# Kernel tuning notes

Measured on AMD Instinct MI355X. Metric: run time of the kernel, lower is better.

The kernel has to match this reference:

```python
import jax, jax.numpy as jnp
import numpy as np

N_NODES = 20000
N_EDGES = 160000
B = 200      # num graphs (nodes per graph = 100)
T = 8        # num_tau
A = 10       # action_size
H = 4        # heads
D = 128      # out_channels
R = 4        # num_relations
NCOS = 64


def rgat(x, edge_index, edge_type, W, q, k, b):
    # W: [R, in, H*D]; q, k: [H*D, H]; b: [D]
    xw = jnp.einsum('ni,rio->nro', x, W)              # [N, R, H*D]
    src, dst = edge_index[0], edge_index[1]
    xj = xw[src, edge_type]                            # [E, H*D] gather by edge + relation
    xi = xw[dst, edge_type]                            # [E, H*D]
    alpha = jax.nn.leaky_relu(xi @ q + xj @ k, 0.2)    # [E, H]
    amax = jax.ops.segment_max(alpha, dst, num_segments=N_NODES)
    ex = jnp.exp(alpha - amax[dst])                    # segment softmax over dst
    denom = jax.ops.segment_sum(ex, dst, num_segments=N_NODES)
    a = ex / denom[dst]                                # [E, H]
    msg = (a[:, :, None] * xj.reshape(-1, H, D)).reshape(-1, H * D)
    agg = jax.ops.segment_sum(msg, dst, num_segments=N_NODES).reshape(-1, H, D)
    return agg.mean(axis=1) + b                        # concat=False -> mean over heads


def noisy_linear(z, w, bias, sw, sb, ew, eb):
    # torch convention: w [out, in]
    return z @ (w + sw * ew).T + (bias + sb * eb)


def setup_inputs():
    key = jax.random.key(0)
    ks = jax.random.split(key, 48)
    def rn(i, shape, scale=0.05):
        return jax.random.normal(ks[i], shape, dtype=jnp.float32) * scale
    SIG = 0.017
    inp = {
        'x': jax.random.normal(ks[0], (N_NODES, 2), dtype=jnp.float32),
        'edge_index': jax.random.randint(ks[1], (2, N_EDGES), 0, N_NODES, dtype=jnp.int32),
        'edge_type': jax.random.randint(ks[2], (N_EDGES,), 0, R, dtype=jnp.int32),
        'taus': jax.random.uniform(ks[3], (B, T, 1), dtype=jnp.float32),
        'W1': rn(4, (R, 2, H * D), 0.3), 'q1': rn(5, (H * D, H), 0.05), 'k1': rn(6, (H * D, H), 0.05), 'b1': rn(7, (D,)),
        'W2': rn(8, (R, D, H * D), 0.06), 'q2': rn(9, (H * D, H), 0.05), 'k2': rn(10, (H * D, H), 0.05), 'b2': rn(11, (D,)),
        'cos_w': rn(12, (D, NCOS), 0.1), 'cos_b': rn(13, (D,)),
        'ff1_w': rn(14, (D, D), 0.1), 'ff1_b': rn(15, (D,)),
        'ff1_sw': jnp.full((D, D), SIG, jnp.float32), 'ff1_sb': jnp.full((D,), SIG, jnp.float32),
        'ff1_ew': rn(16, (D, D), 1.0), 'ff1_eb': rn(17, (D,), 1.0),
        'ff2_w': rn(18, (D, D), 0.1), 'ff2_b': rn(19, (D,)),
        'ff2_sw': jnp.full((D, D), SIG, jnp.float32), 'ff2_sb': jnp.full((D,), SIG, jnp.float32),
        'ff2_ew': rn(20, (D, D), 1.0), 'ff2_eb': rn(21, (D,), 1.0),
        'adv_w': rn(22, (A, D), 0.1), 'adv_b': rn(23, (A,)),
        'adv_sw': jnp.full((A, D), SIG, jnp.float32), 'adv_sb': jnp.full((A,), SIG, jnp.float32),
        'adv_ew': rn(24, (A, D), 1.0), 'adv_eb': rn(25, (A,), 1.0),
        'val_w': rn(26, (1, D), 0.1), 'val_b': rn(27, (1,)),
        'val_sw': jnp.full((1, D), SIG, jnp.float32), 'val_sb': jnp.full((1,), SIG, jnp.float32),
        'val_ew': rn(28, (1, D), 1.0), 'val_eb': rn(29, (1,), 1.0),
    }
    return inp


def reference(x, edge_index, edge_type, taus,
              W1, q1, k1, b1, W2, q2, k2, b2, cos_w, cos_b,
              ff1_w, ff1_b, ff1_sw, ff1_sb, ff1_ew, ff1_eb,
              ff2_w, ff2_b, ff2_sw, ff2_sb, ff2_ew, ff2_eb,
              adv_w, adv_b, adv_sw, adv_sb, adv_ew, adv_eb,
              val_w, val_b, val_sw, val_sb, val_ew, val_eb):
    h = jax.nn.selu(rgat(x, edge_index, edge_type, W1, q1, k1, b1))
    h = jax.nn.selu(rgat(h, edge_index, edge_type, W2, q2, k2, b2))
    g = h.reshape(B, N_NODES // B, D).sum(axis=1)      # global_add_pool (block batch_idx)
    pis = jnp.pi * jnp.arange(1, NCOS + 1, dtype=jnp.float32)  # [NCOS]
    cos = jnp.cos(taus * pis)                           # [B, T, NCOS]
    cos_x = jax.nn.relu(cos @ cos_w.T + cos_b)          # [B, T, D]
    z = (g[:, None, :] * cos_x).reshape(B * T, D)
    z = jax.nn.selu(noisy_linear(z, ff1_w, ff1_b, ff1_sw, ff1_sb, ff1_ew, ff1_eb))
    z = jax.nn.selu(noisy_linear(z, ff2_w, ff2_b, ff2_sw, ff2_sb, ff2_ew, ff2_eb))
    adv = noisy_linear(z, adv_w, adv_b, adv_sw, adv_sb, adv_ew, adv_eb)   # [B*T, A]
    val = noisy_linear(z, val_w, val_b, val_sw, val_sb, val_ew, val_eb)   # [B*T, 1]
    out = val + adv - adv.mean(axis=1, keepdims=True)
    return out.reshape(B, T, A), taus
```

## Files before the change

### kernel.cpp

```cpp
#include <hip/hip_runtime.h>
#include <hip/hip_bf16.h>

constexpr long NN = 20000;
constexpr long NE = 160000;
constexpr long BB = 200;
constexpr long TT = 8;
constexpr long GN = 100;

constexpr long O_FLAG = 0;
constexpr long O_X    = 16;                 constexpr long N_X   = 40000;
constexpr long O_TAU  = O_X + N_X;          constexpr long N_TAU = 1600;
constexpr long O_W1   = O_TAU + N_TAU;      constexpr long N_W1  = 4096;
constexpr long O_Q1   = O_W1 + N_W1;        constexpr long N_Q   = 2048;
constexpr long O_K1   = O_Q1 + N_Q;
constexpr long O_B1   = O_K1 + N_Q;         constexpr long N_B   = 128;
constexpr long O_W2   = O_B1 + N_B;         constexpr long N_W2  = 262144;
constexpr long O_Q2   = O_W2 + N_W2;
constexpr long O_K2   = O_Q2 + N_Q;
constexpr long O_B2   = O_K2 + N_Q;
constexpr long O_CW   = O_B2 + N_B;         constexpr long N_CW  = 8192;
constexpr long O_CB   = O_CW + N_CW;
constexpr long O_F1W  = O_CB + N_B;         constexpr long N_FW  = 16384;
constexpr long O_F1B  = O_F1W + N_FW;
constexpr long O_F1SW = O_F1B + N_B;
constexpr long O_F1SB = O_F1SW + N_FW;
constexpr long O_F1EW = O_F1SB + N_B;
constexpr long O_F1EB = O_F1EW + N_FW;
constexpr long O_F2W  = O_F1EB + N_B;
constexpr long O_F2B  = O_F2W + N_FW;
constexpr long O_F2SW = O_F2B + N_B;
constexpr long O_F2SB = O_F2SW + N_FW;
constexpr long O_F2EW = O_F2SB + N_B;
constexpr long O_F2EB = O_F2EW + N_FW;
constexpr long O_AW   = O_F2EB + N_B;       constexpr long N_AW  = 1280;
constexpr long O_AB   = O_AW + N_AW;        constexpr long N_AB  = 16;
constexpr long O_ASW  = O_AB + N_AB;
constexpr long O_ASB  = O_ASW + N_AW;
constexpr long O_AEW  = O_ASB + N_AB;
constexpr long O_AEB  = O_AEW + N_AW;
constexpr long O_VW   = O_AEB + N_AB;       constexpr long N_VW  = 128;
constexpr long O_VB   = O_VW + N_VW;        constexpr long N_VB  = 16;
constexpr long O_VSW  = O_VB + N_VB;
constexpr long O_VSB  = O_VSW + N_VW;
constexpr long O_VEW  = O_VSB + N_VB;
constexpr long O_VEB  = O_VEW + N_VW;
constexpr long O_WQ1  = O_VEB + N_VB;
constexpr long O_WK1  = O_WQ1 + 32;
constexpr long O_WQ2  = O_WK1 + 32;
constexpr long O_WK2  = O_WQ2 + 2048;
constexpr long O_CF1W = O_WK2 + 2048;
constexpr long O_CF1B = O_CF1W + N_FW;
constexpr long O_CF2W = O_CF1B + N_B;
constexpr long O_CF2B = O_CF2W + N_FW;
constexpr long O_CAW  = O_CF2B + N_B;
constexpr long O_CAB  = O_CAW + N_AW;
constexpr long O_CVW  = O_CAB + N_AB;
constexpr long O_CVB  = O_CVW + N_VW;
constexpr long O_AL1  = O_CVB + N_VB;
constexpr long O_AL2  = O_AL1 + NE*4;
constexpr long O_H1   = O_AL2 + NE*4;
constexpr long O_H2   = O_H1 + NN*128;
constexpr long O_G    = O_H2 + NN*128;
constexpr long O_Z0   = O_G + BB*128;
constexpr long O_Z1   = O_Z0 + BB*TT*128;
constexpr long O_Z2   = O_Z1 + BB*TT*128;
constexpr long O_AGG1 = O_Z2 + BB*TT*128;
constexpr long O_DEG  = O_AGG1;
constexpr long O_CUR  = O_DEG + NN;
constexpr long O_ROWP = O_CUR + NN;
constexpr long O_PERM = O_ROWP + NN + 8;
constexpr long O_XW2  = O_AGG1 + NN*128 + NN*128 + NN*16;
constexpr long O_END_TABLE = O_XW2 + (NN*4*512)/2;
constexpr long MPAD   = 20096;
constexpr long O_H1B  = O_END_TABLE;
constexpr long O_W2BT = O_H1B + (MPAD*128)/2;
constexpr long O_END2 = O_W2BT + (2048L*128)/2;
constexpr long O_AQ   = O_END2;
constexpr long O_AK   = O_AQ + NN*16;
constexpr long O_END3 = O_AK + NN*16;

#define DEVFN __device__ __forceinline__

typedef __attribute__((ext_vector_type(8))) short bf16x8;
typedef __attribute__((ext_vector_type(4))) float f32x4;
typedef __attribute__((ext_vector_type(8))) unsigned short u16x8;

DEVFN float selu_f(float x){ return 1.0507009873554805f * (x > 0.f ? x : 1.6732632423543772f * expm1f(x)); }
DEVFN float lrelu_f(float x){ return x >= 0.f ? x : 0.2f * x; }
DEVFN float bf2f(unsigned short u){ return __uint_as_float(((unsigned)u) << 16); }
DEVFN float wred_max(float v){
    #pragma unroll
    for (int off = 32; off > 0; off >>= 1) v = fmaxf(v, __shfl_xor(v, off));
    return v;
}
DEVFN float wred_sum(float v){
    #pragma unroll
    for (int off = 32; off > 0; off >>= 1) v += __shfl_xor(v, off);
    return v;
}
DEVFN unsigned short f2bfu(float x){
    __hip_bfloat16 b = __float2bfloat16(x);
    return *(unsigned short*)&b;
}

__global__ void k_pre(const unsigned short* taus_u16, const int* ei, float* ws){
    if (blockIdx.x == 0){
        if (threadIdx.x == 0){
            int bf = 1;
            for (int i = 0; i < 128; i++) if (taus_u16[i] > 0x3F80u){ bf = 0; break; }
            ((int*)ws)[0] = bf;
        }
        return;
    }
    long e = (long)(blockIdx.x - 1)*blockDim.x + threadIdx.x;
    if (e >= NE) return;
    atomicAdd((int*)(ws + O_DEG) + ei[NE + e], 1);
}

__global__ void k_scan(float* ws){
    const int* deg = (const int*)(ws + O_DEG);
    int* rowp = (int*)(ws + O_ROWP);
    __shared__ int part[256];
    int tid = threadIdx.x;
    int base = tid * 79;
    int n = 0; if (base < NN) n = min(79, (int)NN - base);
    int s = 0;
    for (int i = 0; i < n; i++) s += deg[base + i];
    part[tid] = s;
    __syncthreads();
    if (tid == 0){
        int acc = 0;
        for (int i = 0; i < 256; i++){ int t = part[i]; part[i] = acc; acc += t; }
    }
    __syncthreads();
    int acc = part[tid];
    for (int i = 0; i < n; i++){ rowp[base + i] = acc; acc += deg[base + i]; }
    if (tid == 0) rowp[NN] = (int)NE;
}

struct ConvArgs { const void* src[38]; long off[38]; int n[38]; };

__global__ void k_conv_scatter(ConvArgs a, const int* ei, float* ws){
    int y = blockIdx.y;
    if (y == 38){
        long e = (long)blockIdx.x*blockDim.x + threadIdx.x;
        if (e >= NE) return;
        int dst = ei[NE + e];
        int pos = atomicAdd((int*)(ws + O_CUR) + dst, 1);
        ((int*)(ws + O_PERM))[((const int*)(ws + O_ROWP))[dst] + pos] = (int)e;
        return;
    }
    long off = a.off[y];
    if (off < 0) return;
    const void* s = a.src[y];
    int n = a.n[y];
    int bf = ((const int*)ws)[0];
    for (int i = blockIdx.x*blockDim.x + threadIdx.x; i < n; i += gridDim.x*blockDim.x){
        float v;
        if (bf){ unsigned short u = ((const unsigned short*)s)[i]; v = bf2f(u); }
        else   { v = ((const float*)s)[i]; }
        ws[off + i] = v;
    }
}

__global__ void k_prep(float* ws){
    int phase = blockIdx.y;
    int idx = blockIdx.x*blockDim.x + threadIdx.x;
    if (phase == 0){
        if (idx >= 4160) return;
        long wsrc, qsrc, dst; int ri, h;
        if (idx < 64){
            int t = idx & 31; h = t & 3; ri = t >> 2;
            wsrc = O_W1 + (long)ri*512;
            qsrc = (idx < 32) ? O_Q1 : O_K1;
            dst  = ((idx < 32) ? O_WQ1 : O_WK1) + t;
        } else {
            int t = (idx - 64) & 2047; h = t & 3; ri = t >> 2;
            wsrc = O_W2 + (long)ri*512;
            qsrc = (idx < 2112) ? O_Q2 : O_K2;
            dst  = ((idx < 2112) ? O_WQ2 : O_WK2) + t;
        }
        const float* W = ws + wsrc;
        const float* Q = ws + qsrc;
        float s = 0.f;
        for (int o = 0; o < 512; o++) s += W[o] * Q[o*4 + h];
        ws[dst] = s;
    } else if (phase == 1){
        const long tw[8] = {O_F1W,O_F2W,O_AW,O_VW, O_F1B,O_F2B,O_AB,O_VB};
        const long ts[8] = {O_F1SW,O_F2SW,O_ASW,O_VSW, O_F1SB,O_F2SB,O_ASB,O_VSB};
        const long te[8] = {O_F1EW,O_F2EW,O_AEW,O_VEW, O_F1EB,O_F2EB,O_AEB,O_VEB};
        const long td[8] = {O_CF1W,O_CF2W,O_CAW,O_CVW, O_CF1B,O_CF2B,O_CAB,O_CVB};
        const int  tn[8] = {16384,16384,1280,128, 128,128,10,1};
        const int  tb[8] = {0,16384,32768,34048, 34176,34304,34432,34442};
        int total = 34443;
        for (int i = idx; i < total; i += gridDim.x*blockDim.x){
            int t = 0;
            #pragma unroll
            for (int q = 1; q < 8; q++) if (i >= tb[q]) t = q;
            int j = i - tb[t];
            if (j < tn[t]) ws[td[t] + j] = ws[tw[t] + j] + ws[ts[t] + j]*ws[te[t] + j];
        }
    } else if (phase == 2){
        if (idx >= 262144) return;
        int np = idx & 2047, k = idx >> 11;
        int r = np >> 9, q = np & 511, d = q >> 2, h = q & 3;
        float v = ws[O_W2 + (long)r*65536 + (long)k*512 + h*128 + d];
        ((__hip_bfloat16*)(ws + O_W2BT))[(long)np*128 + k] = __float2bfloat16(v);
    } else {
        if (idx < 6144) ws[O_H1B + (20000L*128)/2 + idx] = 0.f;
    }
}

__global__ __launch_bounds__(256) void k_node1(const int* ei, const int* et, float* ws){
    int wid = threadIdx.x >> 6, lane = threadIdx.x & 63;
    long n = (long)blockIdx.x*4 + wid;
    const int* rowp = (const int*)(ws + O_ROWP);
    const int* perm = (const int*)(ws + O_PERM);
    int e0 = rowp[n], deg = rowp[n+1] - e0;
    float xd0 = ws[O_X + n*2], xd1 = ws[O_X + n*2 + 1];
    bool have = lane < deg;
    float al[4], xs0 = 0.f, xs1 = 0.f; int rt0 = 0;
    float mx[4] = {-3.0e38f,-3.0e38f,-3.0e38f,-3.0e38f};
    if (have){
        int e = perm[e0 + lane]; int src = ei[e]; rt0 = et[e];
        xs0 = ws[O_X + (long)src*2]; xs1 = ws[O_X + (long)src*2 + 1];
        const float* Wq = ws + O_WQ1 + rt0*8;
        const float* Wk = ws + O_WK1 + rt0*8;
        #pragma unroll
        for (int h = 0; h < 4; h++){
            al[h] = lrelu_f(xd0*Wq[h] + xd1*Wq[4+h] + xs0*Wk[h] + xs1*Wk[4+h]);
            mx[h] = al[h];
        }
    }
    for (int j0 = 64; j0 < deg; j0 += 64){
        int j = j0 + lane;
        if (j < deg){
            int e = perm[e0 + j]; int src = ei[e]; int rt = et[e];
            float a0 = ws[O_X + (long)src*2], a1 = ws[O_X + (long)src*2 + 1];
            const float* Wq = ws + O_WQ1 + rt*8;
            const float* Wk = ws + O_WK1 + rt*8;
            #pragma unroll
            for (int h = 0; h < 4; h++)
                mx[h] = fmaxf(mx[h], lrelu_f(xd0*Wq[h] + xd1*Wq[4+h] + a0*Wk[h] + a1*Wk[4+h]));
        }
    }
    #pragma unroll
    for (int h = 0; h < 4; h++) mx[h] = wred_max(mx[h]);
    float s[4][4][2];
    #pragma unroll
    for (int r = 0; r < 4; r++)
        #pragma unroll
        for (int h = 0; h < 4; h++){ s[r][h][0] = 0.f; s[r][h][1] = 0.f; }
    float den[4] = {0.f,0.f,0.f,0.f};
    if (have){
        #pragma unroll
        for (int h = 0; h < 4; h++){
            float ex = expf(al[h] - mx[h]);
            den[h] += ex;
            float c0 = ex*xs0, c1 = ex*xs1;
            #pragma unroll
            for (int r = 0; r < 4; r++){
                if (r == rt0){ s[r][h][0] += c0; s[r][h][1] += c1; }
            }
        }
    }
    for (int j0 = 64; j0 < deg; j0 += 64){
        int j = j0 + lane;
        if (j < deg){
            int e = perm[e0 + j]; int src = ei[e]; int rt = et[e];
            float a0 = ws[O_X + (long)src*2], a1 = ws[O_X + (long)src*2 + 1];
            const float* Wq = ws + O_WQ1 + rt*8;
            const float* Wk = ws + O_WK1 + rt*8;
            #pragma unroll
            for (int h = 0; h < 4; h++){
                float a = lrelu_f(xd0*Wq[h] + xd1*Wq[4+h] + a0*Wk[h] + a1*Wk[4+h]);
                float ex = expf(a - mx[h]);
                den[h] += ex;
                float c0 = ex*a0, c1 = ex*a1;
                #pragma unroll
                for (int r = 0; r < 4; r++){
                    if (r == rt){ s[r][h][0] += c0; s[r][h][1] += c1; }
                }
            }
        }
    }
    #pragma unroll
    for (int h = 0; h < 4; h++) den[h] = wred_sum(den[h]);
    #pragma unroll
    for (int r = 0; r < 4; r++)
        #pragma unroll
        for (int h = 0; h < 4; h++){
            s[r][h][0] = wred_sum(s[r][h][0]);
            s[r][h][1] = wred_sum(s[r][h][1]);
        }
    float rden[4];
    #pragma unroll
    for (int h = 0; h < 4; h++) rden[h] = den[h] > 0.f ? 0.25f/den[h] : 0.f;
    float v0 = 0.f, v1 = 0.f;
    #pragma unroll
    for (int r = 0; r < 4; r++)
        #pragma unroll
        for (int h = 0; h < 4; h++){
            float2 wa = *(const float2*)&ws[O_W1 + r*1024 +       h*128 + lane*2];
            float2 wb = *(const float2*)&ws[O_W1 + r*1024 + 512 + h*128 + lane*2];
            float t0 = s[r][h][0]*rden[h], t1 = s[r][h][1]*rden[h];
            v0 += wa.x*t0 + wb.x*t1;
            v1 += wa.y*t0 + wb.y*t1;
        }
    float2 b2 = *(const float2*)&ws[O_B1 + lane*2];
    float o0 = selu_f(v0 + b2.x), o1 = selu_f(v1 + b2.y);
    unsigned short* p = (unsigned short*)(ws + O_H1B) + n*128 + lane*2;
    ushort2 pk; pk.x = f2bfu(o0); pk.y = f2bfu(o1);
    *(ushort2*)p = pk;
}

__global__ void k_aqk(float* ws){
    __shared__ float wq[128*16];
    __shared__ float wk[128*16];
    __shared__ float hl[16][129];
    int tid = threadIdx.x;
    long nb = (long)blockIdx.x * 16;
    const unsigned short* h1b = (const unsigned short*)(ws + O_H1B);
    #pragma unroll
    for (int c = 0; c < 8; c++){
        int idx = tid + c*256;
        int i = idx >> 4, o = idx & 15;
        int r = o >> 2, h = o & 3;
        wq[i*16 + o] = ws[O_WQ2 + r*512 + i*4 + h];
        wk[i*16 + o] = ws[O_WK2 + r*512 + i*4 + h];
        hl[idx >> 7][idx & 127] = bf2f(h1b[nb*128 + idx]);
    }
    __syncthreads();
    int j = tid >> 4, o = tid & 15;
    float aq = 0.f, ak = 0.f;
    #pragma unroll 4
    for (int i = 0; i < 128; i++){
        float hv = hl[j][i];
        aq += hv * wq[i*16 + o];
        ak += hv * wk[i*16 + o];
    }
    ws[O_AQ + (nb + j)*16 + o] = aq;
    ws[O_AK + (nb + j)*16 + o] = ak;
}

__global__ void k_xw2_mfma(float* ws){
    __shared__ __align__(16) unsigned short Ash[128*128];
    __shared__ __align__(16) unsigned short Bsh[128*128];
    const unsigned short* h1b  = (const unsigned short*)(ws + O_H1B);
    const unsigned short* w2bt = (const unsigned short*)(ws + O_W2BT);
    long bm = (long)blockIdx.x * 128;
    long bn = (long)blockIdx.y * 128;
    int tid = threadIdx.x;
    char* Ac = (char*)Ash; char* Bc = (char*)Bsh;
    #pragma unroll
    for (int i = 0; i < 8; i++){
        int c = tid + i*256;
        int row = c >> 4, kb = (c & 15) * 16;
        int off = row*256 + (kb ^ ((row & 7) << 4));
        *(bf16x8*)(Ac + off) = *(const bf16x8*)&h1b [(bm + row)*128 + (c & 15)*8];
        *(bf16x8*)(Bc + off) = *(const bf16x8*)&w2bt[(bn + row)*128 + (c & 15)*8];
    }
    __syncthreads();
    int w = tid >> 6, lane = tid & 63;
    int wm = (w >> 1) * 64, wn = (w & 1) * 64;
    int r16 = lane & 15, kq = lane >> 4;
    f32x4 acc[4][4] = {};
    #pragma unroll
    for (int ks = 0; ks < 4; ks++){
        int kbyte = ks*64 + kq*16;
        bf16x8 a[4], b[4];
        #pragma unroll
        for (int m = 0; m < 4; m++){
            int row = wm + m*16 + r16;
            a[m] = *(const bf16x8*)(Ac + row*256 + (kbyte ^ ((row & 7) << 4)));
        }
        #pragma unroll
        for (int n = 0; n < 4; n++){
            int row = wn + n*16 + r16;
            b[n] = *(const bf16x8*)(Bc + row*256 + (kbyte ^ ((row & 7) << 4)));
        }
        #pragma unroll
        for (int m = 0; m < 4; m++)
            #pragma unroll
            for (int n = 0; n < 4; n++)
                acc[m][n] = __builtin_amdgcn_mfma_f32_16x16x32_bf16(a[m], b[n], acc[m][n], 0, 0, 0);
    }
    __hip_bfloat16* xb = (__hip_bfloat16*)(ws + O_XW2);
    #pragma unroll
    for (int m = 0; m < 4; m++){
        long gr0 = bm + wm + m*16 + kq*4;
        #pragma unroll
        for (int j = 0; j < 4; j++){
            long gr = gr0 + j;
            if (gr < NN){
                #pragma unroll
                for (int n = 0; n < 4; n++){
                    long gc = bn + wn + n*16 + r16;
                    xb[gr*2048 + gc] = __float2bfloat16(acc[m][n][j]);
                }
            }
        }
    }
}

__global__ __launch_bounds__(256) void k_node2(const int* ei, const int* et, float* ws){
    __shared__ float excs[4][64][4];
    __shared__ int   esrts[4][64];
    int wid = threadIdx.x >> 6, lane = threadIdx.x & 63;
    long n = (long)blockIdx.x*4 + wid;
    const int* rowp = (const int*)(ws + O_ROWP);
    const int* perm = (const int*)(ws + O_PERM);
    int e0 = rowp[n], deg = rowp[n+1] - e0;
    bool have = lane < deg;
    float al[4]; int srt = 0;
    float mx[4] = {-3.0e38f,-3.0e38f,-3.0e38f,-3.0e38f};
    if (have){
        int e = perm[e0 + lane]; int src = ei[e]; int rt = et[e]; srt = src*4 + rt;
        float4 q4 = *(const float4*)&ws[O_AQ + n*16 + rt*4];
        float4 k4 = *(const float4*)&ws[O_AK + (long)src*16 + rt*4];
        al[0] = lrelu_f(q4.x + k4.x); al[1] = lrelu_f(q4.y + k4.y);
        al[2] = lrelu_f(q4.z + k4.z); al[3] = lrelu_f(q4.w + k4.w);
        #pragma unroll
        for (int h = 0; h < 4; h++) mx[h] = al[h];
    }
    for (int j0 = 64; j0 < deg; j0 += 64){
        int j = j0 + lane;
        if (j < deg){
            int e = perm[e0 + j]; int src = ei[e]; int rt = et[e];
            float4 q4 = *(const float4*)&ws[O_AQ + n*16 + rt*4];
            float4 k4 = *(const float4*)&ws[O_AK + (long)src*16 + rt*4];
            mx[0] = fmaxf(mx[0], lrelu_f(q4.x + k4.x));
            mx[1] = fmaxf(mx[1], lrelu_f(q4.y + k4.y));
            mx[2] = fmaxf(mx[2], lrelu_f(q4.z + k4.z));
            mx[3] = fmaxf(mx[3], lrelu_f(q4.w + k4.w));
        }
    }
    #pragma unroll
    for (int h = 0; h < 4; h++) mx[h] = wred_max(mx[h]);
    float den[4] = {0.f,0.f,0.f,0.f};
    if (have){
        #pragma unroll
        for (int h = 0; h < 4; h++){
            float ex = expf(al[h] - mx[h]);
            den[h] += ex;
            excs[wid][lane][h] = ex;
        }
        esrts[wid][lane] = srt;
    }
    for (int j0 = 64; j0 < deg; j0 += 64){
        int j = j0 + lane;
        if (j < deg){
            int e = perm[e0 + j]; int src = ei[e]; int rt = et[e];
            float4 q4 = *(const float4*)&ws[O_AQ + n*16 + rt*4];
            float4 k4 = *(const float4*)&ws[O_AK + (long)src*16 + rt*4];
            den[0] += expf(lrelu_f(q4.x + k4.x) - mx[0]);
            den[1] += expf(lrelu_f(q4.y + k4.y) - mx[1]);
            den[2] += expf(lrelu_f(q4.z + k4.z) - mx[2]);
            den[3] += expf(lrelu_f(q4.w + k4.w) - mx[3]);
        }
    }
    #pragma unroll
    for (int h = 0; h < 4; h++) den[h] = wred_sum(den[h]);
    __syncthreads();
    const unsigned short* xw2 = (const unsigned short*)(ws + O_XW2);
    float a0[4] = {0.f,0.f,0.f,0.f}, a1[4] = {0.f,0.f,0.f,0.f};
    int mdeg = min(deg, 64);
    int j = 0;
    for (; j + 4 <= mdeg; j += 4){
        long s0 = esrts[wid][j], s1 = esrts[wid][j+1], s2 = esrts[wid][j+2], s3 = esrts[wid][j+3];
        u16x8 v0 = *(const u16x8*)(xw2 + s0*512 + lane*8);
        u16x8 v1 = *(const u16x8*)(xw2 + s1*512 + lane*8);
        u16x8 v2 = *(const u16x8*)(xw2 + s2*512 + lane*8);
        u16x8 v3 = *(const u16x8*)(xw2 + s3*512 + lane*8);
        #pragma unroll
        for (int h = 0; h < 4; h++){
            a0[h] += excs[wid][j  ][h]*bf2f(v0[h]); a1[h] += excs[wid][j  ][h]*bf2f(v0[4+h]);
            a0[h] += excs[wid][j+1][h]*bf2f(v1[h]); a1[h] += excs[wid][j+1][h]*bf2f(v1[4+h]);
            a0[h] += excs[wid][j+2][h]*bf2f(v2[h]); a1[h] += excs[wid][j+2][h]*bf2f(v2[4+h]);
            a0[h] += excs[wid][j+3][h]*bf2f(v3[h]); a1[h] += excs[wid][j+3][h]*bf2f(v3[4+h]);
        }
    }
    for (; j < mdeg; j++){
        long sr = esrts[wid][j];
        u16x8 v = *(const u16x8*)(xw2 + sr*512 + lane*8);
        #pragma unroll
        for (int h = 0; h < 4; h++){
            a0[h] += excs[wid][j][h]*bf2f(v[h]);
            a1[h] += excs[wid][j][h]*bf2f(v[4+h]);
        }
    }
    for (j = 64; j < deg; j++){
        int e = perm[e0 + j]; int src = ei[e]; int rt = et[e];
        float4 q4 = *(const float4*)&ws[O_AQ + n*16 + rt*4];
        float4 k4 = *(const float4*)&ws[O_AK + (long)src*16 + rt*4];
        float ex[4];
        ex[0] = expf(lrelu_f(q4.x + k4.x) - mx[0]);
        ex[1] = expf(lrelu_f(q4.y + k4.y) - mx[1]);
        ex[2] = expf(lrelu_f(q4.z + k4.z) - mx[2]);
        ex[3] = expf(lrelu_f(q4.w + k4.w) - mx[3]);
        u16x8 v = *(const u16x8*)(xw2 + ((long)src*4 + rt)*512 + lane*8);
        #pragma unroll
        for (int h = 0; h < 4; h++){
            a0[h] += ex[h]*bf2f(v[h]);
            a1[h] += ex[h]*bf2f(v[4+h]);
        }
    }
    float rd[4];
    #pragma unroll
    for (int h = 0; h < 4; h++) rd[h] = den[h] > 0.f ? 0.25f/den[h] : 0.f;
    float o0 = a0[0]*rd[0] + a0[1]*rd[1] + a0[2]*rd[2] + a0[3]*rd[3];
    float o1 = a1[0]*rd[0] + a1[1]*rd[1] + a1[2]*rd[2] + a1[3]*rd[3];
    float2 b2 = *(const float2*)&ws[O_B2 + lane*2];
    float2 outv; outv.x = selu_f(o0 + b2.x); outv.y = selu_f(o1 + b2.y);
    *(float2*)&ws[O_H2 + n*128 + lane*2] = outv;
}

__global__ void k_pool(float* ws){
    int b = blockIdx.x, d = threadIdx.x;
    float s = 0.f;
    for (int j = 0; j < GN; j++) s += ws[O_H2 + ((long)b*GN + j)*128 + d];
    ws[O_G + (long)b*128 + d] = s;
}

__global__ void k_tail(float* ws, void* d_out, const void* taus_raw){
    __shared__ float cs[64];
    __shared__ float row0[128], row1[128], row2[128];
    __shared__ float advs[12];
    int bt = blockIdx.x, t = threadIdx.x;
    int b = bt >> 3;
    if (t < 64){
        float tau = ws[O_TAU + bt];
        cs[t] = cosf(tau * (3.14159265358979323846f * (float)(t + 1)));
    }
    __syncthreads();
    {
        const float* cw = ws + O_CW + (long)t*64;
        float s = ws[O_CB + t];
        for (int c = 0; c < 64; c++) s += cs[c]*cw[c];
        s = fmaxf(s, 0.f);
        row0[t] = ws[O_G + (long)b*128 + t] * s;
    }
    __syncthreads();
    {
        const float* W = ws + O_CF1W + (long)t*128;
        float s = ws[O_CF1B + t];
        for (int i = 0; i < 128; i++) s += row0[i]*W[i];
        row1[t] = selu_f(s);
    }
    __syncthreads();
    {
        const float* W = ws + O_CF2W + (long)t*128;
        float s = ws[O_CF2B + t];
        for (int i = 0; i < 128; i++) s += row1[i]*W[i];
        row2[t] = selu_f(s);
    }
    __syncthreads();
    if (t < 11){
        const float* W = (t < 10) ? (ws + O_CAW + (long)t*128) : (ws + O_CVW);
        float s = (t < 10) ? ws[O_CAB + t] : ws[O_CVB];
        for (int i = 0; i < 128; i++) s += row2[i]*W[i];
        advs[t] = s;
    }
    __syncthreads();
    if (t == 0){
        float m = 0.f;
        #pragma unroll
        for (int a = 0; a < 10; a++) m += advs[a];
        m *= 0.1f;
        float val = advs[10];
        int bf = ((const int*)ws)[0];
        if (bf){
            __hip_bfloat16* out = (__hip_bfloat16*)d_out;
            for (int a = 0; a < 10; a++) out[(long)bt*10 + a] = __float2bfloat16(val + advs[a] - m);
            ((unsigned short*)d_out)[16000 + bt] = ((const unsigned short*)taus_raw)[bt];
        } else {
            float* out = (float*)d_out;
            for (int a = 0; a < 10; a++) out[(long)bt*10 + a] = val + advs[a] - m;
            out[16000 + bt] = ((const float*)taus_raw)[bt];
        }
    }
}

extern "C" void kernel_launch(void* const* d_in, const int* in_sizes, int n_in,
                              void* d_out, int out_size, void* d_ws, size_t ws_size,
                              hipStream_t stream){
    (void)in_sizes; (void)n_in; (void)out_size; (void)ws_size;
    float* ws = (float*)d_ws;
    const int* ei = (const int*)d_in[1];
    const int* et = (const int*)d_in[2];

    hipMemsetAsync(ws + O_DEG, 0, (size_t)(2*NN)*4, stream);

    k_pre<<<626, 256, 0, stream>>>((const unsigned short*)d_in[3], ei, ws);
    k_scan<<<1, 256, 0, stream>>>(ws);

    ConvArgs ca;
    static const long conv_o[38] = {
        O_X, -1, -1, O_TAU, O_W1, O_Q1, O_K1, O_B1, O_W2, O_Q2, O_K2, O_B2, O_CW, O_CB,
        O_F1W, O_F1B, O_F1SW, O_F1SB, O_F1EW, O_F1EB,
        O_F2W, O_F2B, O_F2SW, O_F2SB, O_F2EW, O_F2EB,
        O_AW, O_AB, O_ASW, O_ASB, O_AEW, O_AEB,
        O_VW, O_VB, O_VSW, O_VSB, O_VEW, O_VEB };
    static const int conv_n[38] = {
        40000, 0, 0, 1600, 4096, 2048, 2048, 128, 262144, 2048, 2048, 128, 8192, 128,
        16384, 128, 16384, 128, 16384, 128,
        16384, 128, 16384, 128, 16384, 128,
        1280, 10, 1280, 10, 1280, 10,
        128, 1, 128, 1, 128, 1 };
    for (int i = 0; i < 38; i++){ ca.src[i] = d_in[i]; ca.off[i] = conv_o[i]; ca.n[i] = conv_n[i]; }
    k_conv_scatter<<<dim3(625, 39), 256, 0, stream>>>(ca, ei, ws);

    k_prep<<<dim3(1024, 4), 256, 0, stream>>>(ws);

    k_node1<<<5000, 256, 0, stream>>>(ei, et, ws);

    k_xw2_mfma<<<dim3(157, 16), 256, 0, stream>>>(ws);
    k_aqk<<<1250, 256, 0, stream>>>(ws);
    k_node2<<<5000, 256, 0, stream>>>(ei, et, ws);

    k_pool<<<200, 128, 0, stream>>>(ws);
    k_tail<<<1600, 128, 0, stream>>>(ws, d_out, d_in[3]);
}
```

Baseline: 260.6 us.

## Map 16 lanes per node in RGAT node kernels instead of one wavefront

Both node aggregation kernels now process 16 nodes per 256-thread block, with 16 lanes per node instead of a full 64-lane wave. Average in-degree is about 8, so most lanes of a wave sat idle before. In layer 1 the per-relation sums go into shared-memory atomics instead of register arrays plus full-wave reductions. In layer 2 the softmax normalisation is folded into the per-edge weights, and each lane accumulates 8 output dims from wider row loads. The cost is more work per lane, shared atomics, and reliance on wave-synchronous ordering of shared memory with no explicit barriers.

```diff
diff --git a/kernel.cpp b/kernel.cpp
--- a/kernel.cpp
+++ b/kernel.cpp
@@ -88,19 +88,19 @@
 DEVFN float selu_f(float x){ return 1.0507009873554805f * (x > 0.f ? x : 1.6732632423543772f * expm1f(x)); }
 DEVFN float lrelu_f(float x){ return x >= 0.f ? x : 0.2f * x; }
 DEVFN float bf2f(unsigned short u){ return __uint_as_float(((unsigned)u) << 16); }
-DEVFN float wred_max(float v){
-    #pragma unroll
-    for (int off = 32; off > 0; off >>= 1) v = fmaxf(v, __shfl_xor(v, off));
-    return v;
-}
-DEVFN float wred_sum(float v){
-    #pragma unroll
-    for (int off = 32; off > 0; off >>= 1) v += __shfl_xor(v, off);
-    return v;
-}
 DEVFN unsigned short f2bfu(float x){
     __hip_bfloat16 b = __float2bfloat16(x);
     return *(unsigned short*)&b;
+}
+DEVFN float g16_max(float v){
+    #pragma unroll
+    for (int off = 8; off > 0; off >>= 1) v = fmaxf(v, __shfl_xor(v, off));
+    return v;
+}
+DEVFN float g16_sum(float v){
+    #pragma unroll
+    for (int off = 8; off > 0; off >>= 1) v += __shfl_xor(v, off);
+    return v;
 }
 
 __global__ void k_pre(const unsigned short* taus_u16, const int* ei, float* ws){
@@ -212,17 +212,20 @@
 }
 
 __global__ __launch_bounds__(256) void k_node1(const int* ei, const int* et, float* ws){
-    int wid = threadIdx.x >> 6, lane = threadIdx.x & 63;
-    long n = (long)blockIdx.x*4 + wid;
+    __shared__ float sacc[16][32];
+    int tid = threadIdx.x;
+    int g = tid >> 4, t = tid & 15;
+    long n = (long)blockIdx.x*16 + g;
+    sacc[g][t] = 0.f; sacc[g][t + 16] = 0.f;
     const int* rowp = (const int*)(ws + O_ROWP);
     const int* perm = (const int*)(ws + O_PERM);
     int e0 = rowp[n], deg = rowp[n+1] - e0;
     float xd0 = ws[O_X + n*2], xd1 = ws[O_X + n*2 + 1];
-    bool have = lane < deg;
+    bool have = t < deg;
     float al[4], xs0 = 0.f, xs1 = 0.f; int rt0 = 0;
     float mx[4] = {-3.0e38f,-3.0e38f,-3.0e38f,-3.0e38f};
     if (have){
-        int e = perm[e0 + lane]; int src = ei[e]; rt0 = et[e];
+        int e = perm[e0 + t]; int src = ei[e]; rt0 = et[e];
         xs0 = ws[O_X + (long)src*2]; xs1 = ws[O_X + (long)src*2 + 1];
         const float* Wq = ws + O_WQ1 + rt0*8;
         const float* Wk = ws + O_WK1 + rt0*8;
@@ -232,8 +235,8 @@
             mx[h] = al[h];
         }
     }
-    for (int j0 = 64; j0 < deg; j0 += 64){
-        int j = j0 + lane;
+    for (int j0 = 16; j0 < deg; j0 += 16){
+        int j = j0 + t;
         if (j < deg){
             int e = perm[e0 + j]; int src = ei[e]; int rt = et[e];
             float a0 = ws[O_X + (long)src*2], a1 = ws[O_X + (long)src*2 + 1];
@@ -245,27 +248,19 @@
         }
     }
     #pragma unroll
-    for (int h = 0; h < 4; h++) mx[h] = wred_max(mx[h]);
-    float s[4][4][2];
-    #pragma unroll
-    for (int r = 0; r < 4; r++)
-        #pragma unroll
-        for (int h = 0; h < 4; h++){ s[r][h][0] = 0.f; s[r][h][1] = 0.f; }
+    for (int h = 0; h < 4; h++) mx[h] = g16_max(mx[h]);
     float den[4] = {0.f,0.f,0.f,0.f};
     if (have){
         #pragma unroll
         for (int h = 0; h < 4; h++){
             float ex = expf(al[h] - mx[h]);
-            den[h] += ex;
-            float c0 = ex*xs0, c1 = ex*xs1;
-            #pragma unroll
-            for (int r = 0; r < 4; r++){
-                if (r == rt0){ s[r][h][0] += c0; s[r][h][1] += c1; }
-            }
-        }
-    }
-    for (int j0 = 64; j0 < deg; j0 += 64){
-        int j = j0 + lane;
+            den[h] = ex;
+            atomicAdd(&sacc[g][rt0*8 + h*2 + 0], ex*xs0);
+            atomicAdd(&sacc[g][rt0*8 + h*2 + 1], ex*xs1);
+        }
+    }
+    for (int j0 = 16; j0 < deg; j0 += 16){
+        int j = j0 + t;
         if (j < deg){
             int e = perm[e0 + j]; int src = ei[e]; int rt = et[e];
             float a0 = ws[O_X + (long)src*2], a1 = ws[O_X + (long)src*2 + 1];
@@ -276,42 +271,41 @@
                 float a = lrelu_f(xd0*Wq[h] + xd1*Wq[4+h] + a0*Wk[h] + a1*Wk[4+h]);
                 float ex = expf(a - mx[h]);
                 den[h] += ex;
-                float c0 = ex*a0, c1 = ex*a1;
-                #pragma unroll
-                for (int r = 0; r < 4; r++){
-                    if (r == rt){ s[r][h][0] += c0; s[r][h][1] += c1; }
-                }
+                atomicAdd(&sacc[g][rt*8 + h*2 + 0], ex*a0);
+                atomicAdd(&sacc[g][rt*8 + h*2 + 1], ex*a1);
             }
         }
     }
     #pragma unroll
-    for (int h = 0; h < 4; h++) den[h] = wred_sum(den[h]);
+    for (int h = 0; h < 4; h++) den[h] = g16_sum(den[h]);
+    float rden[4];
+    #pragma unroll
+    for (int h = 0; h < 4; h++) rden[h] = den[h] > 0.f ? 0.25f/den[h] : 0.f;
+    float v[8];
+    #pragma unroll
+    for (int k = 0; k < 8; k++) v[k] = 0.f;
     #pragma unroll
     for (int r = 0; r < 4; r++)
         #pragma unroll
         for (int h = 0; h < 4; h++){
-            s[r][h][0] = wred_sum(s[r][h][0]);
-            s[r][h][1] = wred_sum(s[r][h][1]);
-        }
-    float rden[4];
-    #pragma unroll
-    for (int h = 0; h < 4; h++) rden[h] = den[h] > 0.f ? 0.25f/den[h] : 0.f;
-    float v0 = 0.f, v1 = 0.f;
-    #pragma unroll
-    for (int r = 0; r < 4; r++)
-        #pragma unroll
-        for (int h = 0; h < 4; h++){
-            float2 wa = *(const float2*)&ws[O_W1 + r*1024 +       h*128 + lane*2];
-            float2 wb = *(const float2*)&ws[O_W1 + r*1024 + 512 + h*128 + lane*2];
-            float t0 = s[r][h][0]*rden[h], t1 = s[r][h][1]*rden[h];
-            v0 += wa.x*t0 + wb.x*t1;
-            v1 += wa.y*t0 + wb.y*t1;
-        }
-    float2 b2 = *(const float2*)&ws[O_B1 + lane*2];
-    float o0 = selu_f(v0 + b2.x), o1 = selu_f(v1 + b2.y);
-    unsigned short* p = (unsigned short*)(ws + O_H1B) + n*128 + lane*2;
-    ushort2 pk; pk.x = f2bfu(o0); pk.y = f2bfu(o1);
-    *(ushort2*)p = pk;
+            float t0 = sacc[g][r*8 + h*2 + 0]*rden[h];
+            float t1 = sacc[g][r*8 + h*2 + 1]*rden[h];
+            const float4* w0 = (const float4*)&ws[O_W1 + r*1024 +       h*128 + t*8];
+            const float4* w1 = (const float4*)&ws[O_W1 + r*1024 + 512 + h*128 + t*8];
+            float4 wa0 = w0[0], wa1 = w0[1], wb0 = w1[0], wb1 = w1[1];
+            v[0] += wa0.x*t0 + wb0.x*t1;  v[1] += wa0.y*t0 + wb0.y*t1;
+            v[2] += wa0.z*t0 + wb0.z*t1;  v[3] += wa0.w*t0 + wb0.w*t1;
+            v[4] += wa1.x*t0 + wb1.x*t1;  v[5] += wa1.y*t0 + wb1.y*t1;
+            v[6] += wa1.z*t0 + wb1.z*t1;  v[7] += wa1.w*t0 + wb1.w*t1;
+        }
+    float4 ba = *(const float4*)&ws[O_B1 + t*8];
+    float4 bb = *(const float4*)&ws[O_B1 + t*8 + 4];
+    u16x8 pk;
+    pk[0] = f2bfu(selu_f(v[0] + ba.x)); pk[1] = f2bfu(selu_f(v[1] + ba.y));
+    pk[2] = f2bfu(selu_f(v[2] + ba.z)); pk[3] = f2bfu(selu_f(v[3] + ba.w));
+    pk[4] = f2bfu(selu_f(v[4] + bb.x)); pk[5] = f2bfu(selu_f(v[5] + bb.y));
+    pk[6] = f2bfu(selu_f(v[6] + bb.z)); pk[7] = f2bfu(selu_f(v[7] + bb.w));
+    *(u16x8*)((unsigned short*)(ws + O_H1B) + n*128 + t*8) = pk;
 }
 
 __global__ void k_aqk(float* ws){
@@ -404,18 +398,19 @@
 }
 
 __global__ __launch_bounds__(256) void k_node2(const int* ei, const int* et, float* ws){
-    __shared__ float excs[4][64][4];
-    __shared__ int   esrts[4][64];
-    int wid = threadIdx.x >> 6, lane = threadIdx.x & 63;
-    long n = (long)blockIdx.x*4 + wid;
+    __shared__ float exs[16][16][4];
+    __shared__ int   srts[16][16];
+    int tid = threadIdx.x;
+    int g = tid >> 4, t = tid & 15;
+    long n = (long)blockIdx.x*16 + g;
     const int* rowp = (const int*)(ws + O_ROWP);
     const int* perm = (const int*)(ws + O_PERM);
     int e0 = rowp[n], deg = rowp[n+1] - e0;
-    bool have = lane < deg;
+    bool have = t < deg;
     float al[4]; int srt = 0;
     float mx[4] = {-3.0e38f,-3.0e38f,-3.0e38f,-3.0e38f};
     if (have){
-        int e = perm[e0 + lane]; int src = ei[e]; int rt = et[e]; srt = src*4 + rt;
+        int e = perm[e0 + t]; int src = ei[e]; int rt = et[e]; srt = src*4 + rt;
         float4 q4 = *(const float4*)&ws[O_AQ + n*16 + rt*4];
         float4 k4 = *(const float4*)&ws[O_AK + (long)src*16 + rt*4];
         al[0] = lrelu_f(q4.x + k4.x); al[1] = lrelu_f(q4.y + k4.y);
@@ -423,8 +418,8 @@
         #pragma unroll
         for (int h = 0; h < 4; h++) mx[h] = al[h];
     }
-    for (int j0 = 64; j0 < deg; j0 += 64){
-        int j = j0 + lane;
+    for (int j0 = 16; j0 < deg; j0 += 16){
+        int j = j0 + t;
         if (j < deg){
             int e = perm[e0 + j]; int src = ei[e]; int rt = et[e];
             float4 q4 = *(const float4*)&ws[O_AQ + n*16 + rt*4];
@@ -436,19 +431,15 @@
         }
     }
     #pragma unroll
-    for (int h = 0; h < 4; h++) mx[h] = wred_max(mx[h]);
+    for (int h = 0; h < 4; h++) mx[h] = g16_max(mx[h]);
     float den[4] = {0.f,0.f,0.f,0.f};
+    float ex[4] = {0.f,0.f,0.f,0.f};
     if (have){
         #pragma unroll
-        for (int h = 0; h < 4; h++){
-            float ex = expf(al[h] - mx[h]);
-            den[h] += ex;
-            excs[wid][lane][h] = ex;
-        }
-        esrts[wid][lane] = srt;
-    }
-    for (int j0 = 64; j0 < deg; j0 += 64){
-        int j = j0 + lane;
+        for (int h = 0; h < 4; h++){ ex[h] = expf(al[h] - mx[h]); den[h] = ex[h]; }
+    }
+    for (int j0 = 16; j0 < deg; j0 += 16){
+        int j = j0 + t;
         if (j < deg){
             int e = perm[e0 + j]; int src = ei[e]; int rt = et[e];
             float4 q4 = *(const float4*)&ws[O_AQ + n*16 + rt*4];
@@ -460,59 +451,63 @@
         }
     }
     #pragma unroll
-    for (int h = 0; h < 4; h++) den[h] = wred_sum(den[h]);
-    __syncthreads();
+    for (int h = 0; h < 4; h++) den[h] = g16_sum(den[h]);
+    float rd[4];
+    #pragma unroll
+    for (int h = 0; h < 4; h++) rd[h] = den[h] > 0.f ? 0.25f/den[h] : 0.f;
+    if (have){
+        exs[g][t][0] = ex[0]*rd[0]; exs[g][t][1] = ex[1]*rd[1];
+        exs[g][t][2] = ex[2]*rd[2]; exs[g][t][3] = ex[3]*rd[3];
+        srts[g][t] = srt;
+    }
     const unsigned short* xw2 = (const unsigned short*)(ws + O_XW2);
-    float a0[4] = {0.f,0.f,0.f,0.f}, a1[4] = {0.f,0.f,0.f,0.f};
-    int mdeg = min(deg, 64);
-    int j = 0;
-    for (; j + 4 <= mdeg; j += 4){
-        long s0 = esrts[wid][j], s1 = esrts[wid][j+1], s2 = esrts[wid][j+2], s3 = esrts[wid][j+3];
-        u16x8 v0 = *(const u16x8*)(xw2 + s0*512 + lane*8);
-        u16x8 v1 = *(const u16x8*)(xw2 + s1*512 + lane*8);
-        u16x8 v2 = *(const u16x8*)(xw2 + s2*512 + lane*8);
-        u16x8 v3 = *(const u16x8*)(xw2 + s3*512 + lane*8);
-        #pragma unroll
-        for (int h = 0; h < 4; h++){
-            a0[h] += excs[wid][j  ][h]*bf2f(v0[h]); a1[h] += excs[wid][j  ][h]*bf2f(v0[4+h]);
-            a0[h] += excs[wid][j+1][h]*bf2f(v1[h]); a1[h] += excs[wid][j+1][h]*bf2f(v1[4+h]);
-            a0[h] += excs[wid][j+2][h]*bf2f(v2[h]); a1[h] += excs[wid][j+2][h]*bf2f(v2[4+h]);
-            a0[h] += excs[wid][j+3][h]*bf2f(v3[h]); a1[h] += excs[wid][j+3][h]*bf2f(v3[4+h]);
-        }
-    }
-    for (; j < mdeg; j++){
-        long sr = esrts[wid][j];
-        u16x8 v = *(const u16x8*)(xw2 + sr*512 + lane*8);
-        #pragma unroll
-        for (int h = 0; h < 4; h++){
-            a0[h] += excs[wid][j][h]*bf2f(v[h]);
-            a1[h] += excs[wid][j][h]*bf2f(v[4+h]);
-        }
-    }
-    for (j = 64; j < deg; j++){
+    float acc[8];
+    #pragma unroll
+    for (int k = 0; k < 8; k++) acc[k] = 0.f;
+    int mdeg = min(deg, 16);
+    for (int j = 0; j < mdeg; j++){
+        float4 a4 = *(const float4*)exs[g][j];
+        long sr = srts[g][j];
+        const u16x8* row = (const u16x8*)(xw2 + sr*512 + t*32);
+        u16x8 v0 = row[0], v1 = row[1], v2 = row[2], v3 = row[3];
+        acc[0] += a4.x*bf2f(v0[0]) + a4.y*bf2f(v0[1]) + a4.z*bf2f(v0[2]) + a4.w*bf2f(v0[3]);
+        acc[1] += a4.x*bf2f(v0[4]) + a4.y*bf2f(v0[5]) + a4.z*bf2f(v0[6]) + a4.w*bf2f(v0[7]);
+        acc[2] += a4.x*bf2f(v1[0]) + a4.y*bf2f(v1[1]) + a4.z*bf2f(v1[2]) + a4.w*bf2f(v1[3]);
+        acc[3] += a4.x*bf2f(v1[4]) + a4.y*bf2f(v1[5]) + a4.z*bf2f(v1[6]) + a4.w*bf2f(v1[7]);
+        acc[4] += a4.x*bf2f(v2[0]) + a4.y*bf2f(v2[1]) + a4.z*bf2f(v2[2]) + a4.w*bf2f(v2[3]);
+        acc[5] += a4.x*bf2f(v2[4]) + a4.y*bf2f(v2[5]) + a4.z*bf2f(v2[6]) + a4.w*bf2f(v2[7]);
+        acc[6] += a4.x*bf2f(v3[0]) + a4.y*bf2f(v3[1]) + a4.z*bf2f(v3[2]) + a4.w*bf2f(v3[3]);
+        acc[7] += a4.x*bf2f(v3[4]) + a4.y*bf2f(v3[5]) + a4.z*bf2f(v3[6]) + a4.w*bf2f(v3[7]);
+    }
+    for (int j = 16; j < deg; j++){
         int e = perm[e0 + j]; int src = ei[e]; int rt = et[e];
         float4 q4 = *(const float4*)&ws[O_AQ + n*16 + rt*4];
         float4 k4 = *(const float4*)&ws[O_AK + (long)src*16 + rt*4];
-        float ex[4];
-        ex[0] = expf(lrelu_f(q4.x + k4.x) - mx[0]);
-        ex[1] = expf(lrelu_f(q4.y + k4.y) - mx[1]);
-        ex[2] = expf(lrelu_f(q4.z + k4.z) - mx[2]);
-        ex[3] = expf(lrelu_f(q4.w + k4.w) - mx[3]);
-        u16x8 v = *(const u16x8*)(xw2 + ((long)src*4 + rt)*512 + lane*8);
-        #pragma unroll
-        for (int h = 0; h < 4; h++){
-            a0[h] += ex[h]*bf2f(v[h]);
-            a1[h] += ex[h]*bf2f(v[4+h]);
-        }
-    }
-    float rd[4];
-    #pragma unroll
-    for (int h = 0; h < 4; h++) rd[h] = den[h] > 0.f ? 0.25f/den[h] : 0.f;
-    float o0 = a0[0]*rd[0] + a0[1]*rd[1] + a0[2]*rd[2] + a0[3]*rd[3];
-    float o1 = a1[0]*rd[0] + a1[1]*rd[1] + a1[2]*rd[2] + a1[3]*rd[3];
-    float2 b2 = *(const float2*)&ws[O_B2 + lane*2];
-    float2 outv; outv.x = selu_f(o0 + b2.x); outv.y = selu_f(o1 + b2.y);
-    *(float2*)&ws[O_H2 + n*128 + lane*2] = outv;
+        float4 a4;
+        a4.x = expf(lrelu_f(q4.x + k4.x) - mx[0])*rd[0];
+        a4.y = expf(lrelu_f(q4.y + k4.y) - mx[1])*rd[1];
+        a4.z = expf(lrelu_f(q4.z + k4.z) - mx[2])*rd[2];
+        a4.w = expf(lrelu_f(q4.w + k4.w) - mx[3])*rd[3];
+        const u16x8* row = (const u16x8*)(xw2 + ((long)src*4 + rt)*512 + t*32);
+        u16x8 v0 = row[0], v1 = row[1], v2 = row[2], v3 = row[3];
+        acc[0] += a4.x*bf2f(v0[0]) + a4.y*bf2f(v0[1]) + a4.z*bf2f(v0[2]) + a4.w*bf2f(v0[3]);
+        acc[1] += a4.x*bf2f(v0[4]) + a4.y*bf2f(v0[5]) + a4.z*bf2f(v0[6]) + a4.w*bf2f(v0[7]);
+        acc[2] += a4.x*bf2f(v1[0]) + a4.y*bf2f(v1[1]) + a4.z*bf2f(v1[2]) + a4.w*bf2f(v1[3]);
+        acc[3] += a4.x*bf2f(v1[4]) + a4.y*bf2f(v1[5]) + a4.z*bf2f(v1[6]) + a4.w*bf2f(v1[7]);
+        acc[4] += a4.x*bf2f(v2[0]) + a4.y*bf2f(v2[1]) + a4.z*bf2f(v2[2]) + a4.w*bf2f(v2[3]);
+        acc[5] += a4.x*bf2f(v2[4]) + a4.y*bf2f(v2[5]) + a4.z*bf2f(v2[6]) + a4.w*bf2f(v2[7]);
+        acc[6] += a4.x*bf2f(v3[0]) + a4.y*bf2f(v3[1]) + a4.z*bf2f(v3[2]) + a4.w*bf2f(v3[3]);
+        acc[7] += a4.x*bf2f(v3[4]) + a4.y*bf2f(v3[5]) + a4.z*bf2f(v3[6]) + a4.w*bf2f(v3[7]);
+    }
+    float4 ba = *(const float4*)&ws[O_B2 + t*8];
+    float4 bb = *(const float4*)&ws[O_B2 + t*8 + 4];
+    float4 o0, o1;
+    o0.x = selu_f(acc[0] + ba.x); o0.y = selu_f(acc[1] + ba.y);
+    o0.z = selu_f(acc[2] + ba.z); o0.w = selu_f(acc[3] + ba.w);
+    o1.x = selu_f(acc[4] + bb.x); o1.y = selu_f(acc[5] + bb.y);
+    o1.z = selu_f(acc[6] + bb.z); o1.w = selu_f(acc[7] + bb.w);
+    *(float4*)&ws[O_H2 + n*128 + t*8]     = o0;
+    *(float4*)&ws[O_H2 + n*128 + t*8 + 4] = o1;
 }
 
 __global__ void k_pool(float* ws){
@@ -612,11 +607,11 @@
 
     k_prep<<<dim3(1024, 4), 256, 0, stream>>>(ws);
 
-    k_node1<<<5000, 256, 0, stream>>>(ei, et, ws);
+    k_node1<<<1250, 256, 0, stream>>>(ei, et, ws);
 
     k_xw2_mfma<<<dim3(157, 16), 256, 0, stream>>>(ws);
     k_aqk<<<1250, 256, 0, stream>>>(ws);
-    k_node2<<<5000, 256, 0, stream>>>(ei, et, ws);
+    k_node2<<<1250, 256, 0, stream>>>(ei, et, ws);
 
     k_pool<<<200, 128, 0, stream>>>(ws);
     k_tail<<<1600, 128, 0, stream>>>(ws, d_out, d_in[3]);
```

After: 242.4 us. -7.0%, faster.
